# Optimization experiments

Hardware: AMD Instinct MI355X
Metric: run time of the kernel (lower is better)

Reference implementation:

```python
import jax, jax.numpy as jnp
import numpy as np
from jax import lax

DIM = 1024
N_EXPERTS = 64
TOPK = 8
ROUTE_SCALE = 1.0
B = 262144


def setup_inputs() -> dict:
    key = jax.random.key(0)
    kx, kw, kb = jax.random.split(key, 3)
    x = jax.random.normal(kx, (B, DIM), dtype=jnp.float32)
    # nn.Linear(dim, n_experts): weight [E, dim], bias [E]
    bound = 1.0 / np.sqrt(DIM)
    W = jax.random.uniform(kw, (N_EXPERTS, DIM), minval=-bound, maxval=bound, dtype=jnp.float32)
    b = jax.random.uniform(kb, (N_EXPERTS,), minval=-bound, maxval=bound, dtype=jnp.float32)
    return {"x": x, "W": W, "b": b}


def reference(x, W, b):
    # Router linear: [B, dim] x [dim, E] -> [B, E]
    scores = jnp.einsum("bd,ed->be", x, W) + b
    # score_func == 'softmax' (computed in fp32 as in the torch module)
    probs = jax.nn.softmax(scores.astype(jnp.float32), axis=-1)
    # topk + gather (topk values ARE the gathered original scores)
    weights, indices = lax.top_k(probs, TOPK)            # [B, topk] each
    weights = (weights * ROUTE_SCALE).astype(x.dtype)
    # training-time expert usage histogram (replaces the per-expert python loop)
    expert_usage_count = jnp.zeros((N_EXPERTS,), dtype=jnp.float32).at[indices.reshape(-1)].add(1.0)
    total_tokens = jnp.float32(B * TOPK)
    return weights, indices, expert_usage_count, total_tokens
```

## Files before the change

### kernel.cpp

```cpp
#include <hip/hip_runtime.h>
#include <math.h>

#define NTOK   262144
#define DIM    1024
#define NEXP   64
#define TOPK   8
#define WROWS  64
#define ROWS   256
#define BLK    256
#define BK     32
#define NKC    (DIM / BK)
#define SLICE  16896

#define OFF_IDX ((size_t)NTOK * TOPK)
#define OFF_USE (2 * (size_t)NTOK * TOPK)
#define OFF_TOT (OFF_USE + NEXP)

typedef __attribute__((ext_vector_type(8))) short bf16x8;
typedef __attribute__((ext_vector_type(4))) float f32x4;

union FragU { bf16x8 v; unsigned int u[4]; };

__device__ __forceinline__ bf16x8 pack_bf16(float4 a, float4 b) {
    FragU r;
    r.u[0] = (__float_as_uint(a.x) >> 16) | (__float_as_uint(a.y) & 0xFFFF0000u);
    r.u[1] = (__float_as_uint(a.z) >> 16) | (__float_as_uint(a.w) & 0xFFFF0000u);
    r.u[2] = (__float_as_uint(b.x) >> 16) | (__float_as_uint(b.y) & 0xFFFF0000u);
    r.u[3] = (__float_as_uint(b.z) >> 16) | (__float_as_uint(b.w) & 0xFFFF0000u);
    return r.v;
}

__global__ __launch_bounds__(256) void gate_prep_kernel(const float* __restrict__ W,
                                                        unsigned short* __restrict__ wf,
                                                        float* __restrict__ out) {
    int idx = blockIdx.x * 256 + threadIdx.x;
    int j    = idx & 7;
    int lane = (idx >> 3) & 63;
    int nt   = (idx >> 9) & 3;
    int kc   = idx >> 11;
    int fq = lane >> 4, fr = lane & 15;
    float v = W[(size_t)(nt * 16 + fr) * DIM + kc * BK + fq * 8 + j];
    unsigned int u = __float_as_uint(v);
    u += 0x7FFFu + ((u >> 16) & 1u);
    wf[idx] = (unsigned short)(u >> 16);

    if (blockIdx.x == 0) {
        if (threadIdx.x < NEXP) out[OFF_USE + threadIdx.x] = 0.0f;
        if (threadIdx.x == NEXP) out[OFF_TOT] = (float)((size_t)NTOK * TOPK);
    }
}

__global__ __launch_bounds__(BLK, 2) void gate_kernel(const float* __restrict__ x,
                                                      const unsigned short* __restrict__ wf,
                                                      const float* __restrict__ bias,
                                                      float* __restrict__ out) {
    __shared__ __align__(16) char smem[4 * SLICE];
    __shared__ float hist[NEXP];

    const int tid  = threadIdx.x;
    const int w    = tid >> 6;
    const int lane = tid & 63;
    const int fq   = lane >> 4;
    const int fr   = lane & 15;
    const size_t rowBase = (size_t)blockIdx.x * ROWS;

    if (tid < NEXP) hist[tid] = 0.0f;

    char* myslice = smem + w * SLICE;

    const char* xb = (const char*)(x + (rowBase + (size_t)w * WROWS) * DIM);
    const char* src[8];
#pragma unroll
    for (int i = 0; i < 8; i++) {
        int flat = i * 64 + lane;
        int row = flat >> 3;
        int u = (flat & 7) ^ (row & 7);
        src[i] = xb + (size_t)row * (DIM * 4) + u * 16;
    }

#define STAGE(BUF, kc)                                                            \
    do {                                                                          \
        _Pragma("unroll")                                                         \
        for (int i_ = 0; i_ < 8; i_++)                                            \
            __builtin_amdgcn_global_load_lds(                                     \
                (const __attribute__((address_space(1))) unsigned int*)(src[i_] + (kc) * 128), \
                (__attribute__((address_space(3))) unsigned int*)(myslice + (BUF) * 8192 + i_ * 1024), \
                16, 0, 0);                                                        \
    } while (0)

    int aslot[4][2];
#pragma unroll
    for (int mt = 0; mt < 4; mt++)
#pragma unroll
        for (int h = 0; h < 2; h++)
            aslot[mt][h] = (mt * 16 + fr) * 8 + (((fq * 2 + h) ^ fr) & 7);

    const bf16x8* wfv = (const bf16x8*)wf;

    f32x4 acc[4][4] = {};
    bf16x8 bcur[4];

#pragma unroll
    for (int nt = 0; nt < 4; nt++) bcur[nt] = wfv[(size_t)nt * 64 + lane];
    STAGE(0, 0);

#define GSTEP(kc, BUF, PREF)                                                      \
    {                                                                             \
        bf16x8 bnext[4];                                                          \
        if (PREF) {                                                               \
            _Pragma("unroll")                                                     \
            for (int nt = 0; nt < 4; nt++)                                        \
                bnext[nt] = wfv[(size_t)(((kc) + 1) * 4 + nt) * 64 + lane];       \
            STAGE((BUF) ^ 1, (kc) + 1);                                           \
            asm volatile("s_waitcnt vmcnt(12)" ::: "memory");                     \
        } else {                                                                  \
            asm volatile("s_waitcnt vmcnt(0)" ::: "memory");                      \
        }                                                                         \
        __builtin_amdgcn_sched_barrier(0);                                        \
        const float4* xt = (const float4*)(myslice + (BUF) * 8192);               \
        _Pragma("unroll")                                                         \
        for (int mt = 0; mt < 4; mt++) {                                          \
            bf16x8 af = pack_bf16(xt[aslot[mt][0]], xt[aslot[mt][1]]);            \
            _Pragma("unroll")                                                     \
            for (int nt = 0; nt < 4; nt++)                                        \
                acc[mt][nt] = __builtin_amdgcn_mfma_f32_16x16x32_bf16(af, bcur[nt], acc[mt][nt], 0, 0, 0); \
        }                                                                         \
        if (PREF) {                                                               \
            _Pragma("unroll")                                                     \
            for (int nt = 0; nt < 4; nt++) bcur[nt] = bnext[nt];                  \
        }                                                                         \
    }

    for (int kc = 0; kc < NKC - 2; kc += 2) {
        GSTEP(kc, 0, 1);
        GSTEP(kc + 1, 1, 1);
    }
    GSTEP(NKC - 2, 0, 1);
    GSTEP(NKC - 1, 1, 0);

    float* sw = (float*)myslice;
    float bv[4];
#pragma unroll
    for (int nt = 0; nt < 4; nt++) bv[nt] = bias[nt * 16 + fr];
#pragma unroll
    for (int mt = 0; mt < 4; mt++) {
        int mbase = mt * 16 + fq * 4;
#pragma unroll
        for (int nt = 0; nt < 4; nt++) {
            int n = nt * 16 + fr;
#pragma unroll
            for (int r = 0; r < 4; r++)
                sw[(mbase + r) * 65 + n] = acc[mt][nt][r] + bv[nt];
        }
    }
    __syncthreads();

    {
        const float* rp = (const float*)(smem + (tid >> 6) * SLICE) + (tid & 63) * 65;

        float tv[8]; int ti[8];
#pragma unroll
        for (int k = 0; k < 8; k++) { tv[k] = -1e30f; ti[k] = 0; }

#pragma unroll 4
        for (int e = 0; e < NEXP; e++) {
            float s = rp[e];
#pragma unroll
            for (int k = 7; k >= 1; k--) {
                bool up   = s > tv[k - 1];
                bool here = s > tv[k];
                float nv = up ? tv[k - 1] : (here ? s : tv[k]);
                int   ni = up ? ti[k - 1] : (here ? e : ti[k]);
                tv[k] = nv; ti[k] = ni;
            }
            bool c0 = s > tv[0];
            ti[0] = c0 ? e : ti[0];
            tv[0] = c0 ? s : tv[0];
        }
        float m = tv[0];

        float sum = 0.0f;
#pragma unroll 8
        for (int e = 0; e < NEXP; e++) sum += __expf(rp[e] - m);
        float rinv = 1.0f / sum;

        float wv_[8];
#pragma unroll
        for (int k = 0; k < 8; k++) wv_[k] = __expf(tv[k] - m) * rinv;

        size_t ro = (rowBase + tid) * TOPK;
        *(float4*)(out + ro)     = make_float4(wv_[0], wv_[1], wv_[2], wv_[3]);
        *(float4*)(out + ro + 4) = make_float4(wv_[4], wv_[5], wv_[6], wv_[7]);
        *(float4*)(out + OFF_IDX + ro)     = make_float4((float)ti[0], (float)ti[1], (float)ti[2], (float)ti[3]);
        *(float4*)(out + OFF_IDX + ro + 4) = make_float4((float)ti[4], (float)ti[5], (float)ti[6], (float)ti[7]);
#pragma unroll
        for (int k = 0; k < 8; k++) atomicAdd(&hist[ti[k]], 1.0f);
    }
    __syncthreads();
    if (tid < NEXP) atomicAdd(&out[OFF_USE + tid], hist[tid]);
}

extern "C" void kernel_launch(void* const* d_in, const int* in_sizes, int n_in,
                              void* d_out, int out_size, void* d_ws, size_t ws_size,
                              hipStream_t stream) {
    const float* x    = (const float*)d_in[0];
    const float* W    = (const float*)d_in[1];
    const float* bias = (const float*)d_in[2];
    float* out = (float*)d_out;
    unsigned short* wf = (unsigned short*)d_ws;

    gate_prep_kernel<<<256, 256, 0, stream>>>(W, wf, out);
    gate_kernel<<<NTOK / ROWS, BLK, 0, stream>>>(x, wf, bias, out);
}
```

Measured before the change: 260.2 us.

## Halve rows per block and switch to triple-buffered LDS staging pipeline

Reduces each wave's tile from 64 to 32 rows (128 rows per block) and adds a third LDS buffer so that x tiles are prefetched two k-steps ahead, with adjusted vmcnt waits. This raises the launch-bounds occupancy target from 2 to 3 blocks per CU and deepens the load pipeline to hide HBM latency better. In exchange, each MFMA step has less work per B-fragment load, so W fragments are reloaded twice as often per row. Only half the threads now do the top-k/softmax epilogue, which leaves the other half idle.

```diff
diff --git a/kernel.cpp b/kernel.cpp
--- a/kernel.cpp
+++ b/kernel.cpp
@@ -5,12 +5,13 @@
 #define DIM    1024
 #define NEXP   64
 #define TOPK   8
-#define WROWS  64
-#define ROWS   256
+#define WROWS  32
+#define ROWS   128
 #define BLK    256
 #define BK     32
 #define NKC    (DIM / BK)
-#define SLICE  16896
+#define BUFSZ  4096
+#define SLICE  (3 * BUFSZ)
 
 #define OFF_IDX ((size_t)NTOK * TOPK)
 #define OFF_USE (2 * (size_t)NTOK * TOPK)
@@ -50,7 +51,7 @@
     }
 }
 
-__global__ __launch_bounds__(BLK, 2) void gate_kernel(const float* __restrict__ x,
+__global__ __launch_bounds__(BLK, 3) void gate_kernel(const float* __restrict__ x,
                                                       const unsigned short* __restrict__ wf,
                                                       const float* __restrict__ bias,
                                                       float* __restrict__ out) {
@@ -69,9 +70,9 @@
     char* myslice = smem + w * SLICE;
 
     const char* xb = (const char*)(x + (rowBase + (size_t)w * WROWS) * DIM);
-    const char* src[8];
-#pragma unroll
-    for (int i = 0; i < 8; i++) {
+    const char* src[4];
+#pragma unroll
+    for (int i = 0; i < 4; i++) {
         int flat = i * 64 + lane;
         int row = flat >> 3;
         int u = (flat & 7) ^ (row & 7);
@@ -81,69 +82,74 @@
 #define STAGE(BUF, kc)                                                            \
     do {                                                                          \
         _Pragma("unroll")                                                         \
-        for (int i_ = 0; i_ < 8; i_++)                                            \
+        for (int i_ = 0; i_ < 4; i_++)                                            \
             __builtin_amdgcn_global_load_lds(                                     \
                 (const __attribute__((address_space(1))) unsigned int*)(src[i_] + (kc) * 128), \
-                (__attribute__((address_space(3))) unsigned int*)(myslice + (BUF) * 8192 + i_ * 1024), \
+                (__attribute__((address_space(3))) unsigned int*)(myslice + (BUF) * BUFSZ + i_ * 1024), \
                 16, 0, 0);                                                        \
     } while (0)
 
-    int aslot[4][2];
-#pragma unroll
-    for (int mt = 0; mt < 4; mt++)
+    int aslot[2][2];
+#pragma unroll
+    for (int mt = 0; mt < 2; mt++)
 #pragma unroll
         for (int h = 0; h < 2; h++)
             aslot[mt][h] = (mt * 16 + fr) * 8 + (((fq * 2 + h) ^ fr) & 7);
 
     const bf16x8* wfv = (const bf16x8*)wf;
 
-    f32x4 acc[4][4] = {};
+    f32x4 acc[2][4] = {};
     bf16x8 bcur[4];
 
 #pragma unroll
     for (int nt = 0; nt < 4; nt++) bcur[nt] = wfv[(size_t)nt * 64 + lane];
+    __builtin_amdgcn_sched_barrier(0);
     STAGE(0, 0);
-
-#define GSTEP(kc, BUF, PREF)                                                      \
+    STAGE(1, 1);
+
+#define GSTEP(kc, BUF, SBUF, MODE)                                                \
     {                                                                             \
         bf16x8 bnext[4];                                                          \
-        if (PREF) {                                                               \
+        if ((MODE) >= 1) {                                                        \
             _Pragma("unroll")                                                     \
             for (int nt = 0; nt < 4; nt++)                                        \
                 bnext[nt] = wfv[(size_t)(((kc) + 1) * 4 + nt) * 64 + lane];       \
-            STAGE((BUF) ^ 1, (kc) + 1);                                           \
-            asm volatile("s_waitcnt vmcnt(12)" ::: "memory");                     \
-        } else {                                                                  \
-            asm volatile("s_waitcnt vmcnt(0)" ::: "memory");                      \
+            __builtin_amdgcn_sched_barrier(0);                                    \
         }                                                                         \
+        if ((MODE) == 2) STAGE(SBUF, (kc) + 2);                                   \
+        if ((MODE) == 2)      asm volatile("s_waitcnt vmcnt(12)" ::: "memory");   \
+        else if ((MODE) == 1) asm volatile("s_waitcnt vmcnt(8)" ::: "memory");    \
+        else                  asm volatile("s_waitcnt vmcnt(0)" ::: "memory");    \
         __builtin_amdgcn_sched_barrier(0);                                        \
-        const float4* xt = (const float4*)(myslice + (BUF) * 8192);               \
+        const float4* xt = (const float4*)(myslice + (BUF) * BUFSZ);              \
         _Pragma("unroll")                                                         \
-        for (int mt = 0; mt < 4; mt++) {                                          \
+        for (int mt = 0; mt < 2; mt++) {                                          \
             bf16x8 af = pack_bf16(xt[aslot[mt][0]], xt[aslot[mt][1]]);            \
             _Pragma("unroll")                                                     \
             for (int nt = 0; nt < 4; nt++)                                        \
                 acc[mt][nt] = __builtin_amdgcn_mfma_f32_16x16x32_bf16(af, bcur[nt], acc[mt][nt], 0, 0, 0); \
         }                                                                         \
-        if (PREF) {                                                               \
+        if ((MODE) >= 1) {                                                        \
             _Pragma("unroll")                                                     \
             for (int nt = 0; nt < 4; nt++) bcur[nt] = bnext[nt];                  \
         }                                                                         \
     }
 
-    for (int kc = 0; kc < NKC - 2; kc += 2) {
-        GSTEP(kc, 0, 1);
-        GSTEP(kc + 1, 1, 1);
-    }
-    GSTEP(NKC - 2, 0, 1);
-    GSTEP(NKC - 1, 1, 0);
+#pragma unroll 1
+    for (int t = 0; t < 10; t++) {
+        GSTEP(3 * t,     0, 2, 2);
+        GSTEP(3 * t + 1, 1, 0, 2);
+        GSTEP(3 * t + 2, 2, 1, 2);
+    }
+    GSTEP(30, 0, 0, 1);
+    GSTEP(31, 1, 0, 0);
 
     float* sw = (float*)myslice;
     float bv[4];
 #pragma unroll
     for (int nt = 0; nt < 4; nt++) bv[nt] = bias[nt * 16 + fr];
 #pragma unroll
-    for (int mt = 0; mt < 4; mt++) {
+    for (int mt = 0; mt < 2; mt++) {
         int mbase = mt * 16 + fq * 4;
 #pragma unroll
         for (int nt = 0; nt < 4; nt++) {
@@ -155,8 +161,8 @@
     }
     __syncthreads();
 
-    {
-        const float* rp = (const float*)(smem + (tid >> 6) * SLICE) + (tid & 63) * 65;
+    if (tid < ROWS) {
+        const float* rp = (const float*)(smem + (tid >> 5) * SLICE) + (tid & 31) * 65;
 
         float tv[8]; int ti[8];
 #pragma unroll
```

Measured after the change: 254.5 us. -2.2%, faster.

## Split K across waves with register-resident W fragments and 16-row blocks

Applied to the files above, without the earlier changes.

Each block now handles 16 rows instead of 256. The four waves split the K dimension, and each wave holds its quarter of the bf16 W fragments in registers, which removes the per-step W reloads and the double-buffered pipeline. The x tile is loaded into LDS in one shot, and the per-wave partial sums are reduced through LDS before a top-k and softmax pass that only 16 threads run. This raises the block count and shortens the serial loop, at the cost of more blocks, extra reduction syncs, a W reload per block, and most threads idle in the epilogue.

```diff
diff --git a/kernel.cpp b/kernel.cpp
--- a/kernel.cpp
+++ b/kernel.cpp
@@ -5,12 +5,8 @@
 #define DIM    1024
 #define NEXP   64
 #define TOPK   8
-#define WROWS  64
-#define ROWS   256
+#define ROWS   16
 #define BLK    256
-#define BK     32
-#define NKC    (DIM / BK)
-#define SLICE  16896
 
 #define OFF_IDX ((size_t)NTOK * TOPK)
 #define OFF_USE (2 * (size_t)NTOK * TOPK)
@@ -39,7 +35,7 @@
     int nt   = (idx >> 9) & 3;
     int kc   = idx >> 11;
     int fq = lane >> 4, fr = lane & 15;
-    float v = W[(size_t)(nt * 16 + fr) * DIM + kc * BK + fq * 8 + j];
+    float v = W[(size_t)(nt * 16 + fr) * DIM + kc * 32 + fq * 8 + j];
     unsigned int u = __float_as_uint(v);
     u += 0x7FFFu + ((u >> 16) & 1u);
     wf[idx] = (unsigned short)(u >> 16);
@@ -54,7 +50,7 @@
                                                       const unsigned short* __restrict__ wf,
                                                       const float* __restrict__ bias,
                                                       float* __restrict__ out) {
-    __shared__ __align__(16) char smem[4 * SLICE];
+    __shared__ __align__(16) char smem[65536];
     __shared__ float hist[NEXP];
 
     const int tid  = threadIdx.x;
@@ -66,97 +62,62 @@
 
     if (tid < NEXP) hist[tid] = 0.0f;
 
-    char* myslice = smem + w * SLICE;
+    const bf16x8* wfv = (const bf16x8*)wf;
+    bf16x8 bfrag[32];
+#pragma unroll
+    for (int j = 0; j < 8; j++)
+#pragma unroll
+        for (int nt = 0; nt < 4; nt++)
+            bfrag[j * 4 + nt] = wfv[(size_t)((w * 8 + j) * 4 + nt) * 64 + lane];
+    __builtin_amdgcn_sched_barrier(0);
 
-    const char* xb = (const char*)(x + (rowBase + (size_t)w * WROWS) * DIM);
-    const char* src[8];
+    const char* xb = (const char*)(x + rowBase * DIM);
 #pragma unroll
-    for (int i = 0; i < 8; i++) {
-        int flat = i * 64 + lane;
-        int row = flat >> 3;
-        int u = (flat & 7) ^ (row & 7);
-        src[i] = xb + (size_t)row * (DIM * 4) + u * 16;
+    for (int i = 0; i < 16; i++) {
+        const char* s = xb + (size_t)i * 4096 + (size_t)w * 1024
+                        + ((lane ^ (i & 7)) * 16);
+        __builtin_amdgcn_global_load_lds(
+            (const __attribute__((address_space(1))) unsigned int*)s,
+            (__attribute__((address_space(3))) unsigned int*)(smem + w * 16384 + i * 1024),
+            16, 0, 2 );
     }
+    asm volatile("s_waitcnt vmcnt(0)" ::: "memory");
+    __builtin_amdgcn_sched_barrier(0);
 
-#define STAGE(BUF, kc)                                                            \
-    do {                                                                          \
-        _Pragma("unroll")                                                         \
-        for (int i_ = 0; i_ < 8; i_++)                                            \
-            __builtin_amdgcn_global_load_lds(                                     \
-                (const __attribute__((address_space(1))) unsigned int*)(src[i_] + (kc) * 128), \
-                (__attribute__((address_space(3))) unsigned int*)(myslice + (BUF) * 8192 + i_ * 1024), \
-                16, 0, 0);                                                        \
-    } while (0)
-
-    int aslot[4][2];
+    const float4* xt = (const float4*)(smem + w * 16384);
+    f32x4 acc[4] = {};
 #pragma unroll
-    for (int mt = 0; mt < 4; mt++)
+    for (int j = 0; j < 8; j++) {
+        int u0 = j * 8 + fq * 2;
+        bf16x8 af = pack_bf16(xt[fr * 64 + (u0 ^ (fr & 7))],
+                              xt[fr * 64 + ((u0 + 1) ^ (fr & 7))]);
 #pragma unroll
-        for (int h = 0; h < 2; h++)
-            aslot[mt][h] = (mt * 16 + fr) * 8 + (((fq * 2 + h) ^ fr) & 7);
-
-    const bf16x8* wfv = (const bf16x8*)wf;
-
-    f32x4 acc[4][4] = {};
-    bf16x8 bcur[4];
-
-#pragma unroll
-    for (int nt = 0; nt < 4; nt++) bcur[nt] = wfv[(size_t)nt * 64 + lane];
-    STAGE(0, 0);
-
-#define GSTEP(kc, BUF, PREF)                                                      \
-    {                                                                             \
-        bf16x8 bnext[4];                                                          \
-        if (PREF) {                                                               \
-            _Pragma("unroll")                                                     \
-            for (int nt = 0; nt < 4; nt++)                                        \
-                bnext[nt] = wfv[(size_t)(((kc) + 1) * 4 + nt) * 64 + lane];       \
-            STAGE((BUF) ^ 1, (kc) + 1);                                           \
-            asm volatile("s_waitcnt vmcnt(12)" ::: "memory");                     \
-        } else {                                                                  \
-            asm volatile("s_waitcnt vmcnt(0)" ::: "memory");                      \
-        }                                                                         \
-        __builtin_amdgcn_sched_barrier(0);                                        \
-        const float4* xt = (const float4*)(myslice + (BUF) * 8192);               \
-        _Pragma("unroll")                                                         \
-        for (int mt = 0; mt < 4; mt++) {                                          \
-            bf16x8 af = pack_bf16(xt[aslot[mt][0]], xt[aslot[mt][1]]);            \
-            _Pragma("unroll")                                                     \
-            for (int nt = 0; nt < 4; nt++)                                        \
-                acc[mt][nt] = __builtin_amdgcn_mfma_f32_16x16x32_bf16(af, bcur[nt], acc[mt][nt], 0, 0, 0); \
-        }                                                                         \
-        if (PREF) {                                                               \
-            _Pragma("unroll")                                                     \
-            for (int nt = 0; nt < 4; nt++) bcur[nt] = bnext[nt];                  \
-        }                                                                         \
-    }
-
-    for (int kc = 0; kc < NKC - 2; kc += 2) {
-        GSTEP(kc, 0, 1);
-        GSTEP(kc + 1, 1, 1);
-    }
-    GSTEP(NKC - 2, 0, 1);
-    GSTEP(NKC - 1, 1, 0);
-
-    float* sw = (float*)myslice;
-    float bv[4];
-#pragma unroll
-    for (int nt = 0; nt < 4; nt++) bv[nt] = bias[nt * 16 + fr];
-#pragma unroll
-    for (int mt = 0; mt < 4; mt++) {
-        int mbase = mt * 16 + fq * 4;
-#pragma unroll
-        for (int nt = 0; nt < 4; nt++) {
-            int n = nt * 16 + fr;
-#pragma unroll
-            for (int r = 0; r < 4; r++)
-                sw[(mbase + r) * 65 + n] = acc[mt][nt][r] + bv[nt];
-        }
+        for (int nt = 0; nt < 4; nt++)
+            acc[nt] = __builtin_amdgcn_mfma_f32_16x16x32_bf16(af, bfrag[j * 4 + nt], acc[nt], 0, 0, 0);
     }
     __syncthreads();
 
-    {
-        const float* rp = (const float*)(smem + (tid >> 6) * SLICE) + (tid & 63) * 65;
+    float* part = (float*)smem;
+#pragma unroll
+    for (int nt = 0; nt < 4; nt++)
+#pragma unroll
+        for (int r = 0; r < 4; r++)
+            part[w * 1024 + (fq * 4 + r) * 64 + nt * 16 + fr] = acc[nt][r];
+    __syncthreads();
+
+    float* scores = (float*)(smem + 16384);
+#pragma unroll
+    for (int it = 0; it < 4; it++) {
+        int idx = tid + it * 256;
+        int e = idx & 63, r = idx >> 6;
+        float s = bias[e] + part[r * 64 + e] + part[1024 + r * 64 + e]
+                + part[2048 + r * 64 + e] + part[3072 + r * 64 + e];
+        scores[r * 65 + e] = s;
+    }
+    __syncthreads();
+
+    if (tid < ROWS) {
+        const float* rp = scores + tid * 65;
 
         float tv[8]; int ti[8];
 #pragma unroll
```

Result: slower. 570.4 us (+119.2%).
